# Kernel tuning notes

Measured on AMD Instinct MI355X. Metric: run time of the kernel, lower is better.

Reference implementation:

```python
import jax, jax.numpy as jnp
import numpy as np

N = 1024      # recurrent neurons
N_IN = 256    # n_inputs
N_OUT = 32    # n_outputs
T = 500       # n_steps
B = 64        # batch_size
D = 8         # n_delays
ALPHA_P = 0.95      # decayconst(tau_p)
ALPHA_MEM = 0.9     # decayconst(tau_mem)
ALPHA_OUT = 0.9     # decayconst(tau_mem_out)
SCALE = 100.0       # SurrGradSpike.scale

@jax.custom_vjp
def spike(x):
    return (x > 0).astype(x.dtype)

def _spike_fwd(x):
    return spike(x), x

def _spike_bwd(x, g):
    return (g / (SCALE * jnp.abs(x) + 1.0) ** 2,)

spike.defvjp(_spike_fwd, _spike_bwd)


def setup_inputs() -> dict:
    key = jax.random.key(0)
    ks = jax.random.split(key, 7)
    inputs = jax.random.normal(ks[0], (B, T, N_IN), jnp.float32)
    w = jax.random.normal(ks[1], (N, N), jnp.float32) * 0.01
    w_in = jax.random.normal(ks[2], (N_IN, N), jnp.float32) * (1.0 / np.sqrt(N_IN))
    w_out = jax.random.normal(ks[3], (N, N_OUT), jnp.float32) * (1.0 / np.sqrt(N))
    w_signs = jnp.where(jax.random.uniform(ks[4], (N,)) < 0.8, 1.0, -1.0).astype(jnp.float32)
    # plasticity parameter per neuron; negative -> depression
    p = jax.random.uniform(ks[5], (N,), jnp.float32, minval=-0.5, maxval=0.5)
    # each synapse (pre e, post o) assigned exactly one delay bucket -> one-hot dmap [D, N, N]
    delay_assign = jax.random.randint(ks[6], (N, N), 0, D)
    dmap = jax.nn.one_hot(delay_assign, D, dtype=jnp.float32).transpose(2, 0, 1)
    delays = jnp.array([1, 2, 4, 8, 16, 32, 64, 128], jnp.int32)
    return dict(inputs=inputs, w=w, w_in=w_in, w_out=w_out,
                w_signs=w_signs, p=p, dmap=dmap, delays=delays)


def reference(inputs, w, w_in, w_out, w_signs, p, dmap, delays):
    dt = inputs.dtype
    h1 = jnp.einsum('btc,cd->tbd', inputs, w_in)                      # [T,B,N]
    static_weights = dmap * (w_signs[:, None] * jnp.abs(w))           # [D,N,N]
    p_depr = (p < 0).astype(dt)                                       # [N]

    mem0 = jnp.zeros((B, N), dt)
    w_p0 = jnp.zeros((B, N), dt)
    spk_rec0 = jnp.zeros((T, B, N), dt)
    p_rec0 = jnp.zeros((T, B, N), dt)

    def step(carry, xs):
        mem, w_p, spk_rec, p_rec = carry
        t, h1_t = xs
        mthr = mem - 1.0
        out = spike(mthr)
        rst = (mthr > 0).astype(dt)
        # torch negative indexing spk_rec[t-1-delays] wraps; wrapped slots are
        # not yet written (still zero), so mod-T indexing is exactly equivalent.
        idx = (t - 1 - delays) % T                                    # [D]
        tmp = spk_rec[idx] * (1.0 + p_rec[idx])                       # [D,B,N]
        syn_p = jnp.einsum('dbe,deo->bo', tmp, static_weights)        # [B,N]
        w_p = w_p * ALPHA_P + out * p * (1.0 + p_depr * w_p)
        spk_rec = spk_rec.at[t].set(out)
        p_rec = p_rec.at[t].set(w_p)
        mem = ALPHA_MEM * mem + h1_t + syn_p - rst
        return (mem, w_p, spk_rec, p_rec), None

    (_, _, spk_rec, _), _ = jax.lax.scan(
        step, (mem0, w_p0, spk_rec0, p_rec0), (jnp.arange(T), h1))

    h2 = jnp.einsum('tbn,no->tbo', spk_rec, w_out)                    # [T,B,O]

    def out_step(o, h):
        o = ALPHA_OUT * o + h
        return o, o

    _, out_rec = jax.lax.scan(out_step, jnp.zeros((B, N_OUT), dt), h2)
    return out_rec.transpose(1, 0, 2)                                 # [B,T,O]
```

## Files before the change

### kernel.cpp

```cpp
#include <hip/hip_runtime.h>
#include <stdint.h>

#define N_NEUR  1024
#define N_INP   256
#define N_OUTC  32
#define T_STEPS 500
#define BATCH   64
#define N_DEL   8
#define NB      (N_NEUR*BATCH)
#define HSLOTS  132
#define CAP     256
#define H1RING  64

__global__ __launch_bounds__(256) void transpose_inp(const float* __restrict__ inp,
                                                     float* __restrict__ inpT) {
    __shared__ float L[N_INP * 64];
    int t = blockIdx.x;
    int tid = threadIdx.x;
    for (int b = 0; b < 64; ++b) {
        float v = inp[((size_t)b * T_STEPS + t) * N_INP + tid];
        L[tid * 64 + (b ^ (tid & 63))] = v;
    }
    __syncthreads();
    int lane = tid & 63;
    int wv   = tid >> 6;
    for (int cc = 0; cc < 64; ++cc) {
        int c = cc * 4 + wv;
        inpT[((size_t)t * N_INP + c) * 64 + lane] = L[c * 64 + (lane ^ (c & 63))];
    }
}

__global__ __launch_bounds__(256) void transpose_win(const float* __restrict__ w_in,
                                                     float* __restrict__ w_inT) {
    int i = blockIdx.x * 256 + threadIdx.x;
    int n = i >> 8, c = i & 255;
    w_inT[i] = w_in[(size_t)c * N_NEUR + n];
}

__global__ __launch_bounds__(64) void build_csr(const float* __restrict__ w,
                                                const float* __restrict__ signs,
                                                const float* __restrict__ dmap,
                                                uint2* __restrict__ recs,
                                                int* __restrict__ cnt) {
    int o = blockIdx.x * 64 + threadIdx.x;
    int d = blockIdx.y;
    int c = 0;
    uint2* seg = recs + ((size_t)o * N_DEL + d) * CAP;
    for (int e = 0; e < N_NEUR; ++e) {
        float m = dmap[((size_t)d * N_NEUR + e) * N_NEUR + o];
        if (m != 0.f) {
            float G = signs[e] * fabsf(w[(size_t)e * N_NEUR + o]);
            if (c < CAP) seg[c] = make_uint2(__float_as_uint(G), (unsigned)(e * 64));
            ++c;
        }
    }
    if (c > CAP) c = CAP;
    int c4 = (c + 3) & ~3;
    for (; c < c4; ++c) seg[c] = make_uint2(0u, 0u);
    cnt[o * N_DEL + d] = c4;
}

__global__ __launch_bounds__(256) void h1_chunk(int t0,
        const float* __restrict__ inpT, const float* __restrict__ w_inT,
        float* __restrict__ h1r) {
    __shared__ float Li[N_INP * 64];
    __shared__ float Lp[4 * 64];
    int s     = t0 + blockIdx.x;
    int ntile = blockIdx.y;
    int tid   = threadIdx.x;
    int lane  = tid & 63;
    int wv    = tid >> 6;
    const float4* src = (const float4*)(inpT + (size_t)s * (N_INP * 64));
    float4* dst = (float4*)Li;
    for (int k = tid; k < (N_INP * 64) / 4; k += 256) dst[k] = src[k];
    __syncthreads();
    for (int nn = 0; nn < 64; ++nn) {
        int n = ntile * 64 + nn;
        float hp = 0.f;
        const float* wr = w_inT + n * N_INP + wv * 64;
#pragma unroll 8
        for (int c2 = 0; c2 < 64; ++c2)
            hp = fmaf(Li[(wv * 64 + c2) * 64 + lane], wr[c2], hp);
        Lp[wv * 64 + lane] = hp;
        __syncthreads();
        if (wv == 0)
            h1r[(size_t)(s & (H1RING - 1)) * NB + n * 64 + lane] =
                Lp[lane] + Lp[64 + lane] + Lp[128 + lane] + Lp[192 + lane];
        __syncthreads();
    }
}

__global__ __launch_bounds__(256) void step_gather(int t0,
        const uint2* __restrict__ recs, const int* __restrict__ cnt,
        const int* __restrict__ delays, const float* __restrict__ histc,
        float* __restrict__ P) {
    __shared__ uint2 Lrec[4 * CAP];
    __shared__ int   off[5];
    int blk  = blockIdx.x;
    int o    = blk >> 1;
    int h    = blk & 1;
    int tid  = threadIdx.x;
    int lane = tid & 63;
    int wv   = __builtin_amdgcn_readfirstlane(tid >> 6);

    if (tid == 0) {
        int s = 0;
        for (int j = 0; j < 4; ++j) { off[j] = s; s += cnt[o * N_DEL + 4 * h + j]; }
        off[4] = s;
    }
    __syncthreads();
    for (int j = 0; j < 4; ++j) {
        const unsigned long long* R =
            (const unsigned long long*)(recs + ((size_t)o * N_DEL + 4 * h + j) * CAP);
        int base = off[j], n = off[j + 1] - base;
        for (int k = tid; k < n; k += 256) {
            unsigned long long v = __builtin_nontemporal_load(&R[k]);
            Lrec[base + k] = make_uint2((unsigned)v, (unsigned)(v >> 32));
        }
    }
    int dpl  = wv >> 1;
    int sidx = wv & 1;
    int j0 = dpl * 2, j1 = j0 + 1;
    int dl0 = __builtin_amdgcn_readfirstlane(delays[4 * h + j0]);
    int dl1 = __builtin_amdgcn_readfirstlane(delays[4 * h + j1]);
    int q  = lane >> 4;
    int bq = lane & 15;
    __syncthreads();

    float4 acc = make_float4(0.f, 0.f, 0.f, 0.f);
#pragma unroll
    for (int seg = 0; seg < 2; ++seg) {
        int j   = seg ? j1 : j0;
        int dl  = seg ? dl1 : dl0;
        int tau = t0 + sidx - 1 - dl;
        if (tau >= 0) {
            const float* hb = histc + (size_t)(tau % HSLOTS) * NB;
            int kb = off[j], ke = off[j + 1];
            int k = kb;
            for (; k + 8 <= ke; k += 8) {
                uint2 ra = Lrec[k + q];
                uint2 rb = Lrec[k + 4 + q];
                float ga = __uint_as_float(ra.x);
                float gb = __uint_as_float(rb.x);
                float4 a = *((const float4*)(hb + ra.y) + bq);
                float4 b = *((const float4*)(hb + rb.y) + bq);
                acc.x = fmaf(ga, a.x, acc.x); acc.y = fmaf(ga, a.y, acc.y);
                acc.z = fmaf(ga, a.z, acc.z); acc.w = fmaf(ga, a.w, acc.w);
                acc.x = fmaf(gb, b.x, acc.x); acc.y = fmaf(gb, b.y, acc.y);
                acc.z = fmaf(gb, b.z, acc.z); acc.w = fmaf(gb, b.w, acc.w);
            }
            if ((ke - kb) & 4) {
                uint2 r = Lrec[ke - 4 + q];
                float g = __uint_as_float(r.x);
                float4 a = *((const float4*)(hb + r.y) + bq);
                acc.x = fmaf(g, a.x, acc.x); acc.y = fmaf(g, a.y, acc.y);
                acc.z = fmaf(g, a.z, acc.z); acc.w = fmaf(g, a.w, acc.w);
            }
        }
    }
    acc.x += __shfl_xor(acc.x, 16); acc.x += __shfl_xor(acc.x, 32);
    acc.y += __shfl_xor(acc.y, 16); acc.y += __shfl_xor(acc.y, 32);
    acc.z += __shfl_xor(acc.z, 16); acc.z += __shfl_xor(acc.z, 32);
    acc.w += __shfl_xor(acc.w, 16); acc.w += __shfl_xor(acc.w, 32);
    if (lane < 16) {
        int dpg = 2 * h + dpl;
        *((float4*)(P + (((size_t)sidx * N_NEUR + o) * 4 + dpg) * 64 + lane * 4)) = acc;
    }
}

__global__ __launch_bounds__(256) void step_point(int t0,
        const float* __restrict__ P, const float* __restrict__ h1r,
        const float* __restrict__ p,
        float* __restrict__ histc, float* __restrict__ mem,
        float* __restrict__ wp_arr, unsigned long long* __restrict__ spk) {
    int i    = blockIdx.x * 256 + threadIdx.x;
    int o    = i >> 6;
    int lane = i & 63;
    float pn = p[o];
    float pd = (pn < 0.f) ? 1.f : 0.f;
    float m = mem[i];
    float w = wp_arr[i];
#pragma unroll
    for (int sidx = 0; sidx < 2; ++sidx) {
        int s = t0 + sidx;
        const float* Pp = P + ((size_t)sidx * N_NEUR + o) * 4 * 64 + lane;
        float syn = Pp[0] + Pp[64] + Pp[128] + Pp[192];
        float h1 = h1r[(size_t)(s & (H1RING - 1)) * NB + i];
        float out = (m - 1.f > 0.f) ? 1.f : 0.f;
        w = w * 0.95f + out * pn * (1.f + pd * w);
        histc[(size_t)(s % HSLOTS) * NB + i] = out * (1.f + w);
        m = 0.9f * m + h1 + syn - out;
        unsigned long long mask = __ballot(out > 0.f);
        if (lane == 0) spk[(size_t)s * N_NEUR + o] = mask;
    }
    mem[i] = m;
    wp_arr[i] = w;
}

__global__ __launch_bounds__(256) void h2_gemm(const unsigned long long* __restrict__ spk,
                                               const float* __restrict__ w_out,
                                               float* __restrict__ h2) {
    int t = blockIdx.x;
    int lane = threadIdx.x & 63;
    int wv   = threadIdx.x >> 6;
    int o0 = wv * 8;
    float acc[8];
#pragma unroll
    for (int j = 0; j < 8; ++j) acc[j] = 0.f;
    for (int n = 0; n < N_NEUR; ++n) {
        unsigned long long mask = spk[(size_t)t * N_NEUR + n];
        float s = (float)((mask >> lane) & 1ULL);
        const float* wr = w_out + n * N_OUTC + o0;
#pragma unroll
        for (int j = 0; j < 8; ++j) acc[j] = fmaf(s, wr[j], acc[j]);
    }
#pragma unroll
    for (int j = 0; j < 8; ++j)
        h2[((size_t)t * BATCH + lane) * N_OUTC + o0 + j] = acc[j];
}

__global__ __launch_bounds__(256) void out_scan(const float* __restrict__ h2,
                                                float* __restrict__ out) {
    int tid = blockIdx.x * 256 + threadIdx.x;
    int o = tid & 31;
    int b = tid >> 5;
    float acc = 0.f;
    for (int t = 0; t < T_STEPS; ++t) {
        acc = 0.9f * acc + h2[((size_t)t * BATCH + b) * N_OUTC + o];
        out[((size_t)b * T_STEPS + t) * N_OUTC + o] = acc;
    }
}

extern "C" void kernel_launch(void* const* d_in, const int* in_sizes, int n_in,
                              void* d_out, int out_size, void* d_ws, size_t ws_size,
                              hipStream_t stream) {
    (void)in_sizes; (void)n_in; (void)out_size; (void)ws_size;
    const float* inputs = (const float*)d_in[0];
    const float* w      = (const float*)d_in[1];
    const float* w_in   = (const float*)d_in[2];
    const float* w_out  = (const float*)d_in[3];
    const float* signs  = (const float*)d_in[4];
    const float* p      = (const float*)d_in[5];
    const float* dmap   = (const float*)d_in[6];
    const int*   delays = (const int*)d_in[7];
    float* out = (float*)d_out;

    float* ws    = (float*)d_ws;
    float* inpT  = ws;
    float* w_inT = inpT + (size_t)T_STEPS * N_INP * 64;
    float* histc = w_inT + (size_t)N_NEUR * N_INP;
    float* h1r   = histc + (size_t)HSLOTS * NB;
    float* mem   = h1r + (size_t)H1RING * NB;
    float* wp    = mem + NB;
    float* h2    = wp + NB;
    int*   cnt   = (int*)(h2 + (size_t)T_STEPS * BATCH * N_OUTC);
    uint2* recs  = (uint2*)(cnt + N_NEUR * N_DEL);
    unsigned long long* spk =
        (unsigned long long*)(recs + (size_t)N_NEUR * N_DEL * CAP);
    float* P     = (float*)(spk + (size_t)T_STEPS * N_NEUR);

    hipMemsetAsync(histc, 0, sizeof(float) * (size_t)HSLOTS * NB, stream);
    hipMemsetAsync(mem, 0, sizeof(float) * (size_t)2 * NB, stream);

    transpose_inp<<<T_STEPS, 256, 0, stream>>>(inputs, inpT);
    transpose_win<<<(N_NEUR * N_INP) / 256, 256, 0, stream>>>(w_in, w_inT);
    build_csr<<<dim3(16, 8), 64, 0, stream>>>(w, signs, dmap, recs, cnt);

    for (int t0 = 0; t0 < T_STEPS; t0 += 2) {
        if ((t0 & (H1RING - 1)) == 0) {
            int ns = T_STEPS - t0; if (ns > H1RING) ns = H1RING;
            h1_chunk<<<dim3(ns, 16), 256, 0, stream>>>(t0, inpT, w_inT, h1r);
        }
        step_gather<<<2 * N_NEUR, 256, 0, stream>>>(t0, recs, cnt, delays, histc, P);
        step_point<<<NB / 256, 256, 0, stream>>>(t0, P, h1r, p, histc, mem, wp, spk);
    }

    h2_gemm<<<T_STEPS, 256, 0, stream>>>(spk, w_out, h2);
    out_scan<<<8, 256, 0, stream>>>(h2, out);
}
```

Before: 8.659 ms.

## Fuse delayed-spike gather and pointwise neuron update into one kernel

Merges step_gather and step_point into a single step_fused kernel. Each 512-thread block now handles one post-neuron across all 8 delay buckets, instead of two 256-thread blocks per neuron. The per-delay partial sums are reduced in shared memory, and the first wave applies the membrane, plasticity and spike update for two time steps. This halves kernel launches per step pair and removes the global P scratch round-trip. In exchange the grid is half as large and three-quarters of each block idles during the pointwise phase.

```diff
diff --git a/kernel.cpp b/kernel.cpp
--- a/kernel.cpp
+++ b/kernel.cpp
@@ -11,6 +11,7 @@
 #define HSLOTS  132
 #define CAP     256
 #define H1RING  64
+#define LREC_MAX 1152
 
 __global__ __launch_bounds__(256) void transpose_inp(const float* __restrict__ inp,
                                                      float* __restrict__ inpT) {
@@ -90,41 +91,51 @@
     }
 }
 
-__global__ __launch_bounds__(256) void step_gather(int t0,
+__global__ __launch_bounds__(512, 8) void step_fused(int t0,
         const uint2* __restrict__ recs, const int* __restrict__ cnt,
-        const int* __restrict__ delays, const float* __restrict__ histc,
-        float* __restrict__ P) {
-    __shared__ uint2 Lrec[4 * CAP];
-    __shared__ int   off[5];
-    int blk  = blockIdx.x;
-    int o    = blk >> 1;
-    int h    = blk & 1;
+        const int* __restrict__ delays, const float* __restrict__ h1r,
+        const float* __restrict__ p,
+        float* __restrict__ histc, float* __restrict__ mem,
+        float* __restrict__ wp_arr, unsigned long long* __restrict__ spk) {
+    __shared__ uint2 Lrec[LREC_MAX];
+    __shared__ int   off[N_DEL + 1];
+    __shared__ float Lg0[4 * 64];
+    __shared__ float Lg1[4 * 64];
+    int o    = blockIdx.x;
     int tid  = threadIdx.x;
     int lane = tid & 63;
     int wv   = __builtin_amdgcn_readfirstlane(tid >> 6);
 
     if (tid == 0) {
         int s = 0;
-        for (int j = 0; j < 4; ++j) { off[j] = s; s += cnt[o * N_DEL + 4 * h + j]; }
-        off[4] = s;
-    }
-    __syncthreads();
-    for (int j = 0; j < 4; ++j) {
+        for (int d = 0; d < N_DEL; ++d) { off[d] = s; s += cnt[o * N_DEL + d]; }
+        off[N_DEL] = s;
+    }
+    __syncthreads();
+    for (int d = 0; d < N_DEL; ++d) {
         const unsigned long long* R =
-            (const unsigned long long*)(recs + ((size_t)o * N_DEL + 4 * h + j) * CAP);
-        int base = off[j], n = off[j + 1] - base;
-        for (int k = tid; k < n; k += 256) {
+            (const unsigned long long*)(recs + ((size_t)o * N_DEL + d) * CAP);
+        int base = off[d], n = off[d + 1] - base;
+        for (int k = tid; k < n; k += 512) {
             unsigned long long v = __builtin_nontemporal_load(&R[k]);
             Lrec[base + k] = make_uint2((unsigned)v, (unsigned)(v >> 32));
         }
     }
-    int dpl  = wv >> 1;
+    int dp   = wv >> 1;
     int sidx = wv & 1;
-    int j0 = dpl * 2, j1 = j0 + 1;
-    int dl0 = __builtin_amdgcn_readfirstlane(delays[4 * h + j0]);
-    int dl1 = __builtin_amdgcn_readfirstlane(delays[4 * h + j1]);
+    int j0 = dp * 2, j1 = j0 + 1;
+    int dl0 = __builtin_amdgcn_readfirstlane(delays[j0]);
+    int dl1 = __builtin_amdgcn_readfirstlane(delays[j1]);
+    float pn = p[o];
+    float pd = (pn < 0.f) ? 1.f : 0.f;
     int q  = lane >> 4;
     int bq = lane & 15;
+
+    int i_pw = o * 64 + lane;
+    float m_pre   = mem[i_pw];
+    float w_pre   = wp_arr[i_pw];
+    float h1_pre0 = h1r[(size_t)(t0 & (H1RING - 1)) * NB + i_pw];
+    float h1_pre1 = h1r[(size_t)((t0 + 1) & (H1RING - 1)) * NB + i_pw];
     __syncthreads();
 
     float4 acc = make_float4(0.f, 0.f, 0.f, 0.f);
@@ -163,38 +174,29 @@
     acc.z += __shfl_xor(acc.z, 16); acc.z += __shfl_xor(acc.z, 32);
     acc.w += __shfl_xor(acc.w, 16); acc.w += __shfl_xor(acc.w, 32);
     if (lane < 16) {
-        int dpg = 2 * h + dpl;
-        *((float4*)(P + (((size_t)sidx * N_NEUR + o) * 4 + dpg) * 64 + lane * 4)) = acc;
-    }
-}
-
-__global__ __launch_bounds__(256) void step_point(int t0,
-        const float* __restrict__ P, const float* __restrict__ h1r,
-        const float* __restrict__ p,
-        float* __restrict__ histc, float* __restrict__ mem,
-        float* __restrict__ wp_arr, unsigned long long* __restrict__ spk) {
-    int i    = blockIdx.x * 256 + threadIdx.x;
-    int o    = i >> 6;
-    int lane = i & 63;
-    float pn = p[o];
-    float pd = (pn < 0.f) ? 1.f : 0.f;
-    float m = mem[i];
-    float w = wp_arr[i];
-#pragma unroll
-    for (int sidx = 0; sidx < 2; ++sidx) {
-        int s = t0 + sidx;
-        const float* Pp = P + ((size_t)sidx * N_NEUR + o) * 4 * 64 + lane;
-        float syn = Pp[0] + Pp[64] + Pp[128] + Pp[192];
-        float h1 = h1r[(size_t)(s & (H1RING - 1)) * NB + i];
-        float out = (m - 1.f > 0.f) ? 1.f : 0.f;
-        w = w * 0.95f + out * pn * (1.f + pd * w);
-        histc[(size_t)(s % HSLOTS) * NB + i] = out * (1.f + w);
-        m = 0.9f * m + h1 + syn - out;
-        unsigned long long mask = __ballot(out > 0.f);
-        if (lane == 0) spk[(size_t)s * N_NEUR + o] = mask;
-    }
-    mem[i] = m;
-    wp_arr[i] = w;
+        float* Lg = sidx ? Lg1 : Lg0;
+        *((float4*)&Lg[dp * 64 + lane * 4]) = acc;
+    }
+    __syncthreads();
+    if (wv == 0) {
+        float m = m_pre;
+        float w = w_pre;
+#pragma unroll
+        for (int sx = 0; sx < 2; ++sx) {
+            int s = t0 + sx;
+            const float* Lg = sx ? Lg1 : Lg0;
+            float syn = Lg[lane] + Lg[64 + lane] + Lg[128 + lane] + Lg[192 + lane];
+            float h1 = sx ? h1_pre1 : h1_pre0;
+            float out = (m - 1.f > 0.f) ? 1.f : 0.f;
+            w = w * 0.95f + out * pn * (1.f + pd * w);
+            histc[(size_t)(s % HSLOTS) * NB + i_pw] = out * (1.f + w);
+            m = 0.9f * m + h1 + syn - out;
+            unsigned long long mask = __ballot(out > 0.f);
+            if (lane == 0) spk[(size_t)s * N_NEUR + o] = mask;
+        }
+        mem[i_pw] = m;
+        wp_arr[i_pw] = w;
+    }
 }
 
 __global__ __launch_bounds__(256) void h2_gemm(const unsigned long long* __restrict__ spk,
@@ -257,7 +259,6 @@
     uint2* recs  = (uint2*)(cnt + N_NEUR * N_DEL);
     unsigned long long* spk =
         (unsigned long long*)(recs + (size_t)N_NEUR * N_DEL * CAP);
-    float* P     = (float*)(spk + (size_t)T_STEPS * N_NEUR);
 
     hipMemsetAsync(histc, 0, sizeof(float) * (size_t)HSLOTS * NB, stream);
     hipMemsetAsync(mem, 0, sizeof(float) * (size_t)2 * NB, stream);
@@ -271,8 +272,8 @@
             int ns = T_STEPS - t0; if (ns > H1RING) ns = H1RING;
             h1_chunk<<<dim3(ns, 16), 256, 0, stream>>>(t0, inpT, w_inT, h1r);
         }
-        step_gather<<<2 * N_NEUR, 256, 0, stream>>>(t0, recs, cnt, delays, histc, P);
-        step_point<<<NB / 256, 256, 0, stream>>>(t0, P, h1r, p, histc, mem, wp, spk);
+        step_fused<<<N_NEUR, 512, 0, stream>>>(t0, recs, cnt, delays, h1r, p,
+                                               histc, mem, wp, spk);
     }
 
     h2_gemm<<<T_STEPS, 256, 0, stream>>>(spk, w_out, h2);
```

Result: no change. 8.578 ms (-0.9%).

## Stage history slot tiles in LDS and gather from shared memory per delay

Applied to the files above, without the earlier changes.

Replaces the per-neuron global-memory gather with a delay-major kernel. Each block streams one history slot through double-buffered LDS tiles of 128 presynaptic rows, and 16 postsynaptic neurons read their sparse weights against the tile, using per-tile CSR offsets computed in build_csr. This swaps scattered global reads of the history buffer for coalesced tile loads reused across many neurons. The cost is that every block reads a whole slot per delay, adds many barriers, and now reads weight records from global instead of LDS.

```diff
diff --git a/kernel.cpp b/kernel.cpp
--- a/kernel.cpp
+++ b/kernel.cpp
@@ -11,6 +11,7 @@
 #define HSLOTS  132
 #define CAP     256
 #define H1RING  64
+#define TROWS   128
 
 __global__ __launch_bounds__(256) void transpose_inp(const float* __restrict__ inp,
                                                      float* __restrict__ inpT) {
@@ -41,7 +42,8 @@
                                                 const float* __restrict__ signs,
                                                 const float* __restrict__ dmap,
                                                 uint2* __restrict__ recs,
-                                                int* __restrict__ cnt) {
+                                                int* __restrict__ cnt,
+                                                int* __restrict__ off2) {
     int o = blockIdx.x * 64 + threadIdx.x;
     int d = blockIdx.y;
     int c = 0;
@@ -56,8 +58,13 @@
     }
     if (c > CAP) c = CAP;
     int c4 = (c + 3) & ~3;
-    for (; c < c4; ++c) seg[c] = make_uint2(0u, 0u);
+    for (; c < c4; ++c) seg[c] = make_uint2(0u, (unsigned)((N_NEUR - 1) * 64));
     cnt[o * N_DEL + d] = c4;
+    int b2 = 0;
+    for (int j = 0; j <= 8; ++j) {
+        while (b2 < c4 && (int)(seg[b2].y >> 6) < j * TROWS) ++b2;
+        off2[((size_t)o * N_DEL + d) * 9 + j] = b2;
+    }
 }
 
 __global__ __launch_bounds__(256) void h1_chunk(int t0,
@@ -90,81 +97,93 @@
     }
 }
 
-__global__ __launch_bounds__(256) void step_gather(int t0,
-        const uint2* __restrict__ recs, const int* __restrict__ cnt,
+__global__ __launch_bounds__(512, 4) void step_dmaj(int t0,
+        const uint2* __restrict__ recs, const int* __restrict__ off2,
         const int* __restrict__ delays, const float* __restrict__ histc,
         float* __restrict__ P) {
-    __shared__ uint2 Lrec[4 * CAP];
-    __shared__ int   off[5];
-    int blk  = blockIdx.x;
-    int o    = blk >> 1;
-    int h    = blk & 1;
+    __shared__ float buf[2][TROWS * 64];
+    __shared__ int   Soff2[16 * 2 * 9];
+    int bid  = blockIdx.x;
+    int sidx = bid & 1;
+    int dp   = (bid >> 1) & 3;
+    int ot   = bid >> 3;
     int tid  = threadIdx.x;
     int lane = tid & 63;
     int wv   = __builtin_amdgcn_readfirstlane(tid >> 6);
-
-    if (tid == 0) {
-        int s = 0;
-        for (int j = 0; j < 4; ++j) { off[j] = s; s += cnt[o * N_DEL + 4 * h + j]; }
-        off[4] = s;
+    int q    = lane >> 4;
+    int bq   = lane & 15;
+
+    for (int i = tid; i < 16 * 2 * 9; i += 512) {
+        int ol = i / 18, rem = i % 18, sg = rem / 9, j = rem % 9;
+        Soff2[i] = off2[(((size_t)(ot * 16 + ol)) * N_DEL + (2 * dp + sg)) * 9 + j];
     }
     __syncthreads();
-    for (int j = 0; j < 4; ++j) {
-        const unsigned long long* R =
-            (const unsigned long long*)(recs + ((size_t)o * N_DEL + 4 * h + j) * CAP);
-        int base = off[j], n = off[j + 1] - base;
-        for (int k = tid; k < n; k += 256) {
-            unsigned long long v = __builtin_nontemporal_load(&R[k]);
-            Lrec[base + k] = make_uint2((unsigned)v, (unsigned)(v >> 32));
-        }
-    }
-    int dpl  = wv >> 1;
-    int sidx = wv & 1;
-    int j0 = dpl * 2, j1 = j0 + 1;
-    int dl0 = __builtin_amdgcn_readfirstlane(delays[4 * h + j0]);
-    int dl1 = __builtin_amdgcn_readfirstlane(delays[4 * h + j1]);
-    int q  = lane >> 4;
-    int bq = lane & 15;
-    __syncthreads();
-
-    float4 acc = make_float4(0.f, 0.f, 0.f, 0.f);
-#pragma unroll
-    for (int seg = 0; seg < 2; ++seg) {
-        int j   = seg ? j1 : j0;
-        int dl  = seg ? dl1 : dl0;
+
+    float4 acc[2];
+    acc[0] = make_float4(0.f, 0.f, 0.f, 0.f);
+    acc[1] = make_float4(0.f, 0.f, 0.f, 0.f);
+
+#pragma unroll
+    for (int sg = 0; sg < 2; ++sg) {
+        int d  = 2 * dp + sg;
+        int dl = __builtin_amdgcn_readfirstlane(delays[d]);
         int tau = t0 + sidx - 1 - dl;
-        if (tau >= 0) {
-            const float* hb = histc + (size_t)(tau % HSLOTS) * NB;
-            int kb = off[j], ke = off[j + 1];
-            int k = kb;
-            for (; k + 8 <= ke; k += 8) {
-                uint2 ra = Lrec[k + q];
-                uint2 rb = Lrec[k + 4 + q];
-                float ga = __uint_as_float(ra.x);
-                float gb = __uint_as_float(rb.x);
-                float4 a = *((const float4*)(hb + ra.y) + bq);
-                float4 b = *((const float4*)(hb + rb.y) + bq);
-                acc.x = fmaf(ga, a.x, acc.x); acc.y = fmaf(ga, a.y, acc.y);
-                acc.z = fmaf(ga, a.z, acc.z); acc.w = fmaf(ga, a.w, acc.w);
-                acc.x = fmaf(gb, b.x, acc.x); acc.y = fmaf(gb, b.y, acc.y);
-                acc.z = fmaf(gb, b.z, acc.z); acc.w = fmaf(gb, b.w, acc.w);
+        if (tau < 0) continue;
+        const float* slot = histc + (size_t)(tau % HSLOTS) * NB;
+        float4 r0, r1, r2, r3;
+        {
+            const float4* src = (const float4*)slot;
+            int base = tid * 4;
+            r0 = src[base]; r1 = src[base + 1]; r2 = src[base + 2]; r3 = src[base + 3];
+        }
+        for (int j = 0; j < 8; ++j) {
+            {
+                float4* B = (float4*)buf[j & 1];
+                int base = tid * 4;
+                B[base] = r0; B[base + 1] = r1; B[base + 2] = r2; B[base + 3] = r3;
             }
-            if ((ke - kb) & 4) {
-                uint2 r = Lrec[ke - 4 + q];
-                float g = __uint_as_float(r.x);
-                float4 a = *((const float4*)(hb + r.y) + bq);
-                acc.x = fmaf(g, a.x, acc.x); acc.y = fmaf(g, a.y, acc.y);
-                acc.z = fmaf(g, a.z, acc.z); acc.w = fmaf(g, a.w, acc.w);
+            __syncthreads();
+            if (j < 7) {
+                const float4* src = (const float4*)(slot + (size_t)(j + 1) * TROWS * 64);
+                int base = tid * 4;
+                r0 = src[base]; r1 = src[base + 1]; r2 = src[base + 2]; r3 = src[base + 3];
             }
-        }
-    }
-    acc.x += __shfl_xor(acc.x, 16); acc.x += __shfl_xor(acc.x, 32);
-    acc.y += __shfl_xor(acc.y, 16); acc.y += __shfl_xor(acc.y, 32);
-    acc.z += __shfl_xor(acc.z, 16); acc.z += __shfl_xor(acc.z, 32);
-    acc.w += __shfl_xor(acc.w, 16); acc.w += __shfl_xor(acc.w, 32);
-    if (lane < 16) {
-        int dpg = 2 * h + dpl;
-        *((float4*)(P + (((size_t)sidx * N_NEUR + o) * 4 + dpg) * 64 + lane * 4)) = acc;
+            const float* LB = buf[j & 1];
+#pragma unroll
+            for (int oi = 0; oi < 2; ++oi) {
+                int ol = wv * 2 + oi;
+                int o  = ot * 16 + ol;
+                int pb = Soff2[(ol * 2 + sg) * 9 + j];
+                int pe = Soff2[(ol * 2 + sg) * 9 + j + 1];
+                const uint2* R = recs + ((size_t)o * N_DEL + d) * CAP;
+#pragma unroll 4
+                for (int k = (pb & ~3); k < pe; k += 4) {
+                    int pos = k + q;
+                    bool v = (pos >= pb) && (pos < pe);
+                    uint2 r = R[v ? pos : pb];
+                    float g = v ? __uint_as_float(r.x) : 0.f;
+                    int ro  = v ? (int)(r.y - (unsigned)(j * TROWS * 64)) : 0;
+                    float4 a = *((const float4*)(LB + ro) + bq);
+                    acc[oi].x = fmaf(g, a.x, acc[oi].x);
+                    acc[oi].y = fmaf(g, a.y, acc[oi].y);
+                    acc[oi].z = fmaf(g, a.z, acc[oi].z);
+                    acc[oi].w = fmaf(g, a.w, acc[oi].w);
+                }
+            }
+            __syncthreads();
+        }
+    }
+#pragma unroll
+    for (int oi = 0; oi < 2; ++oi) {
+        float4 a = acc[oi];
+        a.x += __shfl_xor(a.x, 16); a.x += __shfl_xor(a.x, 32);
+        a.y += __shfl_xor(a.y, 16); a.y += __shfl_xor(a.y, 32);
+        a.z += __shfl_xor(a.z, 16); a.z += __shfl_xor(a.z, 32);
+        a.w += __shfl_xor(a.w, 16); a.w += __shfl_xor(a.w, 32);
+        if (lane < 16) {
+            int o = ot * 16 + wv * 2 + oi;
+            *((float4*)(P + (((size_t)sidx * N_NEUR + o) * 4 + dp) * 64 + lane * 4)) = a;
+        }
     }
 }
 
@@ -257,21 +276,22 @@
     uint2* recs  = (uint2*)(cnt + N_NEUR * N_DEL);
     unsigned long long* spk =
         (unsigned long long*)(recs + (size_t)N_NEUR * N_DEL * CAP);
-    float* P     = (float*)(spk + (size_t)T_STEPS * N_NEUR);
+    int*   off2  = (int*)(spk + (size_t)T_STEPS * N_NEUR);
+    float* P     = (float*)(off2 + (size_t)N_NEUR * N_DEL * 9);
 
     hipMemsetAsync(histc, 0, sizeof(float) * (size_t)HSLOTS * NB, stream);
     hipMemsetAsync(mem, 0, sizeof(float) * (size_t)2 * NB, stream);
 
     transpose_inp<<<T_STEPS, 256, 0, stream>>>(inputs, inpT);
     transpose_win<<<(N_NEUR * N_INP) / 256, 256, 0, stream>>>(w_in, w_inT);
-    build_csr<<<dim3(16, 8), 64, 0, stream>>>(w, signs, dmap, recs, cnt);
+    build_csr<<<dim3(16, 8), 64, 0, stream>>>(w, signs, dmap, recs, cnt, off2);
 
     for (int t0 = 0; t0 < T_STEPS; t0 += 2) {
         if ((t0 & (H1RING - 1)) == 0) {
             int ns = T_STEPS - t0; if (ns > H1RING) ns = H1RING;
             h1_chunk<<<dim3(ns, 16), 256, 0, stream>>>(t0, inpT, w_inT, h1r);
         }
-        step_gather<<<2 * N_NEUR, 256, 0, stream>>>(t0, recs, cnt, delays, histc, P);
+        step_dmaj<<<512, 512, 0, stream>>>(t0, recs, off2, delays, histc, P);
         step_point<<<NB / 256, 256, 0, stream>>>(t0, P, h1r, p, histc, mem, wp, spk);
     }
 
```

New measurement: 18.20 ms. 110% more time.
